# Kernel optimization log

Hardware: AMD Instinct MI355X
Metric: run time of the kernel (lower is better)

Reference implementation:

```python
import jax, jax.numpy as jnp
import numpy as np

NQ = 100000  # Query nodes
NP = 100000  # Product nodes
E = 600000   # edges per relation
D_IN = 128
D_H = 128
# relation r: (src_type, dst_type); 0=Query, 1=Product
# 0: Click Q->P, 1: reverse_Click P->Q, 2: reverse_QueryResult P->Q, 3: QueryResult Q->P
REL = [(0, 1), (1, 0), (1, 0), (0, 1)]
N_NODES = [NQ, NP]


def setup_inputs() -> dict:
    key = jax.random.key(0)
    ks = jax.random.split(key, 12)
    s = 1.0 / np.sqrt(D_IN)  # keep activations well-scaled across 2 layers
    return {
        "x_query": jax.random.normal(ks[0], (NQ, D_IN), jnp.float32),
        "x_product": jax.random.normal(ks[1], (NP, D_IN), jnp.float32),
        "src_idx": jax.random.randint(ks[2], (4, E), 0, NQ, jnp.int32),
        "dst_idx": jax.random.randint(ks[3], (4, E), 0, NP, jnp.int32),
        "W_self1": jax.random.normal(ks[4], (4, D_IN, D_H), jnp.float32) * s,
        "W_neigh1": jax.random.normal(ks[5], (4, D_IN, D_H), jnp.float32) * s,
        "b1": jnp.zeros((4, D_H), jnp.float32),
        "W_self2": jax.random.normal(ks[6], (4, D_H, D_H), jnp.float32) * s,
        "W_neigh2": jax.random.normal(ks[7], (4, D_H, D_H), jnp.float32) * s,
        "b2": jnp.zeros((4, D_H), jnp.float32),
    }


def _hetero_sage_layer(h, W_self, W_neigh, b, src_idx, dst_idx):
    # h: [h_query, h_product]; per-relation SAGEConv(mean), cross-relation sum
    acc = [None, None]
    for r, (s, t) in enumerate(REL):
        nt = N_NODES[t]
        msg = h[s][src_idx[r]]                                   # [E, d] gather
        neigh_sum = jax.ops.segment_sum(msg, dst_idx[r], num_segments=nt)
        deg = jax.ops.segment_sum(jnp.ones((E,), h[s].dtype), dst_idx[r],
                                  num_segments=nt)
        neigh_mean = neigh_sum / jnp.maximum(deg, 1.0)[:, None]
        out = h[t] @ W_self[r] + neigh_mean @ W_neigh[r] + b[r]
        acc[t] = out if acc[t] is None else acc[t] + out
    return acc


def reference(x_query, x_product, src_idx, dst_idx,
              W_self1, W_neigh1, b1, W_self2, W_neigh2, b2):
    h = [x_query, x_product]
    h = _hetero_sage_layer(h, W_self1, W_neigh1, b1, src_idx, dst_idx)
    h = [jax.nn.relu(v) for v in h]  # ReLU only between layers
    h = _hetero_sage_layer(h, W_self2, W_neigh2, b2, src_idx, dst_idx)
    return (h[0], h[1])  # (H_query, H_product)
```

## Files before the change

### kernel.cpp

```cpp
#include <hip/hip_runtime.h>
#include <hip/hip_bf16.h>

#define N_NODES 100000
#define NEDGE   600000
#define SCAN_B  1024
#define NBLK    98
#define BSHIFT  9
#define NBUCK   196
#define BCAP    3456

typedef __attribute__((ext_vector_type(8))) short bf16x8;
typedef __attribute__((ext_vector_type(4))) short s16x4;
typedef __attribute__((ext_vector_type(4))) float f32x4;
typedef __attribute__((ext_vector_type(4))) unsigned u32x4;
typedef __attribute__((ext_vector_type(2))) int int2v;

__device__ __forceinline__ short f2bf(float f) {
  union { float f; unsigned u; } x; x.f = f;
  unsigned r = x.u + 0x7FFFu + ((x.u >> 16) & 1u);
  return (short)(r >> 16);
}

__global__ __launch_bounds__(256) void bin_k(const int* __restrict__ sidx,
                                             const int* __restrict__ didx,
                                             int* __restrict__ bincnt,
                                             int2v* __restrict__ stage) {
  __shared__ int hist[NBUCK];
  __shared__ int base[NBUCK];
  int r = blockIdx.y, t = threadIdx.x;
  int e0 = blockIdx.x * 2048 + t;
  const int* dd = didx + (size_t)r * NEDGE;
  const int* ss = sidx + (size_t)r * NEDGE;
  for (int i = t; i < NBUCK; i += 256) hist[i] = 0;
  __syncthreads();
  int sv[8], dv[8], bu[8], lr[8];
#pragma unroll
  for (int j = 0; j < 8; ++j) {
    int e = e0 + j * 256;
    if (e < NEDGE) {
      dv[j] = dd[e]; sv[j] = ss[e];
      bu[j] = dv[j] >> BSHIFT;
      lr[j] = atomicAdd(&hist[bu[j]], 1);
    }
  }
  __syncthreads();
  for (int i = t; i < NBUCK; i += 256)
    base[i] = atomicAdd(&bincnt[r * NBUCK + i], hist[i]);
  __syncthreads();
#pragma unroll
  for (int j = 0; j < 8; ++j) {
    int e = e0 + j * 256;
    if (e < NEDGE)
      stage[(size_t)(r * NBUCK + bu[j]) * BCAP + base[bu[j]] + lr[j]] =
          (int2v){sv[j], dv[j]};
  }
}

__global__ __launch_bounds__(256) void hist_k(const int2v* __restrict__ stage,
                                              const int* __restrict__ bincnt,
                                              int* __restrict__ cnt) {
  __shared__ int h[512];
  int bu = blockIdx.x, r = blockIdx.y, t = threadIdx.x;
  int len = bincnt[r * NBUCK + bu];
  const int2v* sg = stage + (size_t)(r * NBUCK + bu) * BCAP;
  h[t] = 0; h[t + 256] = 0;
  __syncthreads();
  int lo = bu << BSHIFT;
  for (int i = t; i < len; i += 256) atomicAdd(&h[sg[i].y - lo], 1);
  __syncthreads();
  int d0 = lo + t;
  if (d0 < N_NODES)       cnt[r * N_NODES + d0]       = h[t];
  if (d0 + 256 < N_NODES) cnt[r * N_NODES + d0 + 256] = h[t + 256];
}

__global__ __launch_bounds__(256) void scan1_k(const int* __restrict__ cnt,
                                               int* __restrict__ bsum) {
  __shared__ int lds[256];
  int b = blockIdx.x, r = blockIdx.y, t = threadIdx.x;
  int i0 = b * SCAN_B + t * 4;
  int s = 0;
#pragma unroll
  for (int j = 0; j < 4; ++j)
    if (i0 + j < N_NODES) s += cnt[r * N_NODES + i0 + j];
  lds[t] = s;
  __syncthreads();
  for (int st = 128; st > 0; st >>= 1) {
    if (t < st) lds[t] += lds[t + st];
    __syncthreads();
  }
  if (t == 0) bsum[r * NBLK + b] = lds[0];
}

__global__ __launch_bounds__(128) void scan2_k(int* __restrict__ bsum) {
  __shared__ int buf[128];
  int t = threadIdx.x;
  for (int r = 0; r < 4; ++r) {
    int v = (t < NBLK) ? bsum[r * NBLK + t] : 0;
    buf[t] = v;
    __syncthreads();
    for (int st = 1; st < 128; st <<= 1) {
      int x = (t >= st) ? buf[t - st] : 0;
      __syncthreads();
      buf[t] += x;
      __syncthreads();
    }
    if (t < NBLK) bsum[r * NBLK + t] = buf[t] - v;
    __syncthreads();
  }
}

__global__ __launch_bounds__(256) void scan3_k(const int* __restrict__ cnt,
                                               const int* __restrict__ bsum,
                                               int* __restrict__ off) {
  __shared__ int lds[256];
  int b = blockIdx.x, r = blockIdx.y, t = threadIdx.x;
  int i0 = b * SCAN_B + t * 4;
  int c[4] = {0, 0, 0, 0};
#pragma unroll
  for (int j = 0; j < 4; ++j)
    if (i0 + j < N_NODES) c[j] = cnt[r * N_NODES + i0 + j];
  int s = c[0] + c[1] + c[2] + c[3];
  lds[t] = s;
  __syncthreads();
  for (int st = 1; st < 256; st <<= 1) {
    int x = (t >= st) ? lds[t - st] : 0;
    __syncthreads();
    lds[t] += x;
    __syncthreads();
  }
  int run = bsum[r * NBLK + b] + lds[t] - s;
  int* o = off + r * (N_NODES + 1);
#pragma unroll
  for (int j = 0; j < 4; ++j) {
    if (i0 + j < N_NODES) { o[i0 + j] = run; run += c[j]; }
  }
  if (b == 0 && t == 0) o[N_NODES] = NEDGE;
}

__global__ __launch_bounds__(256) void place_k(const int2v* __restrict__ stage,
                                               const int* __restrict__ bincnt,
                                               const int* __restrict__ off,
                                               int* __restrict__ csr) {
  __shared__ int ofl[512];
  __shared__ int cur[512];
  int bu = blockIdx.x, r = blockIdx.y, t = threadIdx.x;
  int len = bincnt[r * NBUCK + bu];
  const int2v* sg = stage + (size_t)(r * NBUCK + bu) * BCAP;
  const int* of = off + r * (N_NODES + 1);
  int* cs = csr + (size_t)r * NEDGE;
  int lo = bu << BSHIFT;
  int d0 = lo + t;
  ofl[t]       = (d0 < N_NODES) ? of[d0] : 0;
  ofl[t + 256] = (d0 + 256 < N_NODES) ? of[d0 + 256] : 0;
  cur[t] = 0; cur[t + 256] = 0;
  __syncthreads();
  for (int i = t; i < len; i += 256) {
    int2v sd = sg[i];
    int dl = sd.y - lo;
    int pos = ofl[dl] + atomicAdd(&cur[dl], 1);
    cs[pos] = sd.x;
  }
}

__global__ __launch_bounds__(256) void cvt_bf16_k(const float* __restrict__ x,
                                                  unsigned* __restrict__ o) {
  int i = blockIdx.x * 256 + threadIdx.x;
  if (i >= N_NODES * 16) return;
  f32x4 v0 = ((const f32x4*)x)[i * 2];
  f32x4 v1 = ((const f32x4*)x)[i * 2 + 1];
  unsigned r0 = (unsigned)(unsigned short)f2bf(v0[0]) |
                ((unsigned)(unsigned short)f2bf(v0[1]) << 16);
  unsigned r1 = (unsigned)(unsigned short)f2bf(v0[2]) |
                ((unsigned)(unsigned short)f2bf(v0[3]) << 16);
  unsigned r2 = (unsigned)(unsigned short)f2bf(v1[0]) |
                ((unsigned)(unsigned short)f2bf(v1[1]) << 16);
  unsigned r3 = (unsigned)(unsigned short)f2bf(v1[2]) |
                ((unsigned)(unsigned short)f2bf(v1[3]) << 16);
  ((u32x4*)o)[i] = (u32x4){r0, r1, r2, r3};
}

__global__ __launch_bounds__(256) void prep_w_k(const float* __restrict__ Ws1,
                                                const float* __restrict__ Wn1,
                                                const float* __restrict__ Ws2,
                                                const float* __restrict__ Wn2,
                                                short* __restrict__ WTp) {
  int tid = blockIdx.x * 256 + threadIdx.x;
  int lane = tid & 63;
  int n0 = (tid >> 6) & 7;
  int idx3 = tid >> 9;
  int k0 = idx3 % 12;
  int lt = idx3 / 12;
  int l = lt >> 1, t = lt & 1;
  const float* Wself  = l ? Ws2 : Ws1;
  const float* Wneigh = l ? Wn2 : Wn1;
  int rA = t ? 0 : 1, rB = t ? 3 : 2;
  int n = n0 * 16 + (lane & 15);
  int kbase = k0 * 32 + (lane >> 4) * 8;
  short out[8];
#pragma unroll
  for (int j = 0; j < 8; ++j) {
    int k = kbase + j;
    int kk = k & 127, blk = k >> 7;
    float v;
    if (blk == 0)      v = Wself[rA * 16384 + kk * 128 + n] + Wself[rB * 16384 + kk * 128 + n];
    else if (blk == 1) v = Wneigh[rA * 16384 + kk * 128 + n];
    else               v = Wneigh[rB * 16384 + kk * 128 + n];
    out[j] = f2bf(v);
  }
  s16x4* dst = (s16x4*)&WTp[tid * 8];
  dst[0] = *(s16x4*)&out[0];
  dst[1] = *(s16x4*)&out[4];
}

__global__ __launch_bounds__(256) void prep_b_k(const float* __restrict__ b1,
                                                const float* __restrict__ b2,
                                                float* __restrict__ biasc) {
  int tid = blockIdx.x * 256 + threadIdx.x;
  if (tid >= 512) return;
  int l = tid >> 8, t = (tid >> 7) & 1, c = tid & 127;
  const float* b = l ? b2 : b1;
  int rA = t ? 0 : 1, rB = t ? 3 : 2;
  biasc[tid] = b[rA * 128 + c] + b[rB * 128 + c];
}

__global__ __launch_bounds__(256) void gather_mean_k(const unsigned* __restrict__ src,
    const int* __restrict__ csrA, const int* __restrict__ offA,
    const int* __restrict__ csrB, const int* __restrict__ offB,
    unsigned* __restrict__ meanA, unsigned* __restrict__ meanB) {
  int wv = __builtin_amdgcn_readfirstlane(threadIdx.x >> 6);
  int wid = blockIdx.x * 4 + wv;
  int lane = threadIdx.x & 63;
  int n = wid >> 1, rel = wid & 1;
  if (n >= N_NODES) return;
  const int* csr = rel ? csrB : csrA;
  const int* off = rel ? offB : offA;
  unsigned* mean = rel ? meanB : meanA;
  int p0 = off[n], p1 = off[n + 1];
  int deg = p1 - p0;
  int rowg = lane >> 4;
  int colg = lane & 15;
  float a[8] = {};
  for (int p = p0; p < p1; p += 8) {
    int pc0 = p + rowg, pc1 = p + 4 + rowg;
    int i0 = csr[pc0 < p1 ? pc0 : p0];
    int i1 = csr[pc1 < p1 ? pc1 : p0];
    u32x4 u0 = *(const u32x4*)(src + (size_t)i0 * 64 + colg * 4);
    u32x4 u1 = *(const u32x4*)(src + (size_t)i1 * 64 + colg * 4);
    if (pc0 < p1) {
#pragma unroll
      for (int q = 0; q < 4; ++q) {
        union { unsigned w; float f; } lo, hi;
        lo.w = u0[q] << 16; hi.w = u0[q] & 0xffff0000u;
        a[2 * q] += lo.f; a[2 * q + 1] += hi.f;
      }
    }
    if (pc1 < p1) {
#pragma unroll
      for (int q = 0; q < 4; ++q) {
        union { unsigned w; float f; } lo, hi;
        lo.w = u1[q] << 16; hi.w = u1[q] & 0xffff0000u;
        a[2 * q] += lo.f; a[2 * q + 1] += hi.f;
      }
    }
  }
#pragma unroll
  for (int q = 0; q < 8; ++q) {
    a[q] += __shfl_xor(a[q], 16);
    a[q] += __shfl_xor(a[q], 32);
  }
  if (rowg == 0) {
    float inv = 1.0f / (float)(deg > 1 ? deg : 1);
    u32x4 wv4;
#pragma unroll
    for (int q = 0; q < 4; ++q) {
      wv4[q] = (unsigned)(unsigned short)f2bf(a[2 * q] * inv) |
               ((unsigned)(unsigned short)f2bf(a[2 * q + 1] * inv) << 16);
    }
    *(u32x4*)(mean + (size_t)n * 64 + colg * 4) = wv4;
  }
}

template<int OUT_RELU_BF16>
__global__ __launch_bounds__(256) void gemm_k(const short* __restrict__ selfp,
    const short* __restrict__ meanA, const short* __restrict__ meanB,
    const short* __restrict__ WTp, const float* __restrict__ biasc,
    void* __restrict__ outp) {
  __shared__ short Wlds[6 * 8 * 512];
  int tid = threadIdx.x;
  int lane = tid & 63, wave = tid >> 6;
  int rowbase = blockIdx.x * 128 + wave * 32;
  int r0 = rowbase + (lane & 15), r1 = r0 + 16;
  int rc0 = r0 < N_NODES ? r0 : N_NODES - 1;
  int rc1 = r1 < N_NODES ? r1 : N_NODES - 1;
  int kg = lane >> 4;
  f32x4 acc[2][8] = {};
  for (int half = 0; half < 2; ++half) {
    __syncthreads();
    const f32x4* s = (const f32x4*)WTp + half * 3072;
    f32x4* dst = (f32x4*)Wlds;
#pragma unroll
    for (int i = 0; i < 12; ++i) dst[tid + i * 256] = s[tid + i * 256];
    __syncthreads();
    for (int k0h = 0; k0h < 6; ++k0h) {
      int k0 = half * 6 + k0h;
      int kin = (k0 & 3) * 32 + kg * 8;
      const short* mp = (k0 < 4) ? selfp : ((k0 < 8) ? meanA : meanB);
      bf16x8 a0 = *(const bf16x8*)(mp + (size_t)rc0 * 128 + kin);
      bf16x8 a1 = *(const bf16x8*)(mp + (size_t)rc1 * 128 + kin);
      const short* wb = &Wlds[k0h * 4096 + lane * 8];
#pragma unroll
      for (int n0 = 0; n0 < 8; ++n0) {
        bf16x8 b = *(const bf16x8*)(wb + n0 * 512);
        acc[0][n0] = __builtin_amdgcn_mfma_f32_16x16x32_bf16(a0, b, acc[0][n0], 0, 0, 0);
        acc[1][n0] = __builtin_amdgcn_mfma_f32_16x16x32_bf16(a1, b, acc[1][n0], 0, 0, 0);
      }
    }
  }
  int colb = lane & 15, rloc = kg * 4;
#pragma unroll
  for (int mt = 0; mt < 2; ++mt) {
    int rb = rowbase + mt * 16 + rloc;
#pragma unroll
    for (int n0 = 0; n0 < 8; ++n0) {
      int cc = n0 * 16 + colb;
      float bv = biasc[cc];
#pragma unroll
      for (int j = 0; j < 4; ++j) {
        int rr = rb + j;
        if (rr < N_NODES) {
          float v = acc[mt][n0][j] + bv;
          if (OUT_RELU_BF16) {
            ((short*)outp)[(size_t)rr * 128 + cc] = f2bf(v > 0.f ? v : 0.f);
          } else {
            ((float*)outp)[(size_t)rr * 128 + cc] = v;
          }
        }
      }
    }
  }
}

extern "C" void kernel_launch(void* const* d_in, const int* in_sizes, int n_in,
                              void* d_out, int out_size, void* d_ws, size_t ws_size,
                              hipStream_t stream) {
  (void)in_sizes; (void)n_in; (void)out_size; (void)ws_size;
  const float* xq  = (const float*)d_in[0];
  const float* xp  = (const float*)d_in[1];
  const int*   src = (const int*)d_in[2];
  const int*   dst = (const int*)d_in[3];
  const float* Ws1 = (const float*)d_in[4];
  const float* Wn1 = (const float*)d_in[5];
  const float* b1  = (const float*)d_in[6];
  const float* Ws2 = (const float*)d_in[7];
  const float* Wn2 = (const float*)d_in[8];
  const float* b2  = (const float*)d_in[9];

  char* w = (char*)d_ws;
  int*   cnt    = (int*)w;      w += (size_t)4 * N_NODES * 4;
  int*   bincnt = (int*)w;      w += 4096;
  int*   off    = (int*)w;      w += (size_t)4 * (N_NODES + 1) * 4;
  int*   csr    = (int*)w;      w += (size_t)4 * NEDGE * 4;
  short* meanA  = (short*)w;    w += (size_t)N_NODES * 128 * 2;
  short* meanB  = (short*)w;    w += (size_t)N_NODES * 128 * 2;
  short* h1q    = (short*)w;    w += (size_t)N_NODES * 128 * 2;
  short* h1p    = (short*)w;    w += (size_t)N_NODES * 128 * 2;
  short* xqb    = (short*)w;    w += (size_t)N_NODES * 128 * 2;
  short* xpb    = (short*)w;    w += (size_t)N_NODES * 128 * 2;
  short* WTp    = (short*)w;    w += (size_t)4 * 49152 * 2;
  float* biasc  = (float*)w;    w += 512 * 4;
  int*   bsum   = (int*)w;      w += 4 * 128 * 4;
  int2v* stage  = (int2v*)meanA;

  dim3 b256(256);
  const int bgrid = (NEDGE + 2047) / 2048;
  const int ggrid = (N_NODES + 127) / 128;
  const int wgrid = (2 * N_NODES + 3) / 4;
  const int cgrid = (N_NODES * 16 + 255) / 256;
  const int NP1 = N_NODES + 1;

  hipMemsetAsync(bincnt, 0, 4096, stream);
  bin_k<<<dim3(bgrid, 4), b256, 0, stream>>>(src, dst, bincnt, stage);
  hist_k<<<dim3(NBUCK, 4), b256, 0, stream>>>(stage, bincnt, cnt);
  scan1_k<<<dim3(NBLK, 4), b256, 0, stream>>>(cnt, bsum);
  scan2_k<<<dim3(1), dim3(128), 0, stream>>>(bsum);
  scan3_k<<<dim3(NBLK, 4), b256, 0, stream>>>(cnt, bsum, off);
  place_k<<<dim3(NBUCK, 4), b256, 0, stream>>>(stage, bincnt, off, csr);
  prep_w_k<<<dim3(384), b256, 0, stream>>>(Ws1, Wn1, Ws2, Wn2, WTp);
  prep_b_k<<<dim3(2), b256, 0, stream>>>(b1, b2, biasc);
  cvt_bf16_k<<<dim3(cgrid), b256, 0, stream>>>(xq, (unsigned*)xqb);
  cvt_bf16_k<<<dim3(cgrid), b256, 0, stream>>>(xp, (unsigned*)xpb);

  gather_mean_k<<<wgrid, b256, 0, stream>>>((const unsigned*)xpb,
      csr + 1 * NEDGE, off + 1 * NP1, csr + 2 * NEDGE, off + 2 * NP1,
      (unsigned*)meanA, (unsigned*)meanB);
  gemm_k<1><<<ggrid, b256, 0, stream>>>(xqb, meanA, meanB,
      WTp + 0 * 49152, biasc + 0, h1q);

  gather_mean_k<<<wgrid, b256, 0, stream>>>((const unsigned*)xqb,
      csr + 0 * NEDGE, off + 0 * NP1, csr + 3 * NEDGE, off + 3 * NP1,
      (unsigned*)meanA, (unsigned*)meanB);
  gemm_k<1><<<ggrid, b256, 0, stream>>>(xpb, meanA, meanB,
      WTp + 1 * 49152, biasc + 128, h1p);

  gather_mean_k<<<wgrid, b256, 0, stream>>>((const unsigned*)h1p,
      csr + 1 * NEDGE, off + 1 * NP1, csr + 2 * NEDGE, off + 2 * NP1,
      (unsigned*)meanA, (unsigned*)meanB);
  gemm_k<0><<<ggrid, b256, 0, stream>>>(h1q, meanA, meanB,
      WTp + 2 * 49152, biasc + 256, (float*)d_out);

  gather_mean_k<<<wgrid, b256, 0, stream>>>((const unsigned*)h1q,
      csr + 0 * NEDGE, off + 0 * NP1, csr + 3 * NEDGE, off + 3 * NP1,
      (unsigned*)meanA, (unsigned*)meanB);
  gemm_k<0><<<ggrid, b256, 0, stream>>>(h1p, meanA, meanB,
      WTp + 3 * 49152, biasc + 384, (float*)d_out + (size_t)N_NODES * 128);
}
```

Measured before the change: 544.0 us.

## Batch both node types per layer into single gather and GEMM launches

```diff
diff --git a/kernel.cpp b/kernel.cpp
--- a/kernel.cpp
+++ b/kernel.cpp
@@ -162,8 +162,12 @@
   }
 }
 
-__global__ __launch_bounds__(256) void cvt_bf16_k(const float* __restrict__ x,
-                                                  unsigned* __restrict__ o) {
+__global__ __launch_bounds__(256) void cvt2_k(const float* __restrict__ x0,
+                                              const float* __restrict__ x1,
+                                              unsigned* __restrict__ o0,
+                                              unsigned* __restrict__ o1) {
+  const float* x = blockIdx.y ? x1 : x0;
+  unsigned* o = blockIdx.y ? o1 : o0;
   int i = blockIdx.x * 256 + threadIdx.x;
   if (i >= N_NODES * 16) return;
   f32x4 v0 = ((const f32x4*)x)[i * 2];
@@ -223,69 +227,109 @@
   biasc[tid] = b[rA * 128 + c] + b[rB * 128 + c];
 }
 
-__global__ __launch_bounds__(256) void gather_mean_k(const unsigned* __restrict__ src,
-    const int* __restrict__ csrA, const int* __restrict__ offA,
-    const int* __restrict__ csrB, const int* __restrict__ offB,
-    unsigned* __restrict__ meanA, unsigned* __restrict__ meanB) {
+#define ACC8(u, a)                                            \
+  {                                                           \
+    _Pragma("unroll") for (int q = 0; q < 4; ++q) {           \
+      union { unsigned w; float f; } lo_, hi_;                \
+      lo_.w = (u)[q] << 16; hi_.w = (u)[q] & 0xffff0000u;     \
+      (a)[2 * q] += lo_.f; (a)[2 * q + 1] += hi_.f;           \
+    }                                                         \
+  }
+
+__device__ __forceinline__ int clampi(int q, int p0, int p1) {
+  int t = q < p1 ? q : p0;
+  return t < NEDGE ? t : 0;
+}
+
+__global__ __launch_bounds__(256) void gather2_k(
+    const unsigned* __restrict__ src0, const unsigned* __restrict__ src1,
+    const int* __restrict__ csr, const int* __restrict__ off,
+    unsigned* __restrict__ m00, unsigned* __restrict__ m01,
+    unsigned* __restrict__ m10, unsigned* __restrict__ m11) {
   int wv = __builtin_amdgcn_readfirstlane(threadIdx.x >> 6);
   int wid = blockIdx.x * 4 + wv;
   int lane = threadIdx.x & 63;
-  int n = wid >> 1, rel = wid & 1;
-  if (n >= N_NODES) return;
-  const int* csr = rel ? csrB : csrA;
-  const int* off = rel ? offB : offA;
-  unsigned* mean = rel ? meanB : meanA;
-  int p0 = off[n], p1 = off[n + 1];
-  int deg = p1 - p0;
+  int type = wid >= N_NODES;
+  int n = type ? wid - N_NODES : wid;
+  const unsigned* src = type ? src1 : src0;
+  const int* csrA = csr + (type ? 0 : 1) * NEDGE;
+  const int* csrB = csr + (type ? 3 : 2) * NEDGE;
+  const int* offA = off + (type ? 0 : 1) * (N_NODES + 1);
+  const int* offB = off + (type ? 3 : 2) * (N_NODES + 1);
+  unsigned* mA = type ? m10 : m00;
+  unsigned* mB = type ? m11 : m01;
+  int pA0 = offA[n], pA1 = offA[n + 1];
+  int pB0 = offB[n], pB1 = offB[n + 1];
+  int degA = pA1 - pA0, degB = pB1 - pB0;
   int rowg = lane >> 4;
   int colg = lane & 15;
-  float a[8] = {};
-  for (int p = p0; p < p1; p += 8) {
-    int pc0 = p + rowg, pc1 = p + 4 + rowg;
-    int i0 = csr[pc0 < p1 ? pc0 : p0];
-    int i1 = csr[pc1 < p1 ? pc1 : p0];
+  float a[8] = {}, b[8] = {};
+  {
+    int ia0 = csrA[clampi(pA0 + rowg,     pA0, pA1)];
+    int ia1 = csrA[clampi(pA0 + 4 + rowg, pA0, pA1)];
+    int ib0 = csrB[clampi(pB0 + rowg,     pB0, pB1)];
+    int ib1 = csrB[clampi(pB0 + 4 + rowg, pB0, pB1)];
+    u32x4 ua0 = *(const u32x4*)(src + (size_t)ia0 * 64 + colg * 4);
+    u32x4 ua1 = *(const u32x4*)(src + (size_t)ia1 * 64 + colg * 4);
+    u32x4 ub0 = *(const u32x4*)(src + (size_t)ib0 * 64 + colg * 4);
+    u32x4 ub1 = *(const u32x4*)(src + (size_t)ib1 * 64 + colg * 4);
+    if (pA0 + rowg     < pA1) ACC8(ua0, a);
+    if (pA0 + 4 + rowg < pA1) ACC8(ua1, a);
+    if (pB0 + rowg     < pB1) ACC8(ub0, b);
+    if (pB0 + 4 + rowg < pB1) ACC8(ub1, b);
+  }
+  for (int p = pA0 + 8; p < pA1; p += 8) {
+    int i0 = csrA[clampi(p + rowg,     pA0, pA1)];
+    int i1 = csrA[clampi(p + 4 + rowg, pA0, pA1)];
     u32x4 u0 = *(const u32x4*)(src + (size_t)i0 * 64 + colg * 4);
     u32x4 u1 = *(const u32x4*)(src + (size_t)i1 * 64 + colg * 4);
-    if (pc0 < p1) {
-#pragma unroll
-      for (int q = 0; q < 4; ++q) {
-        union { unsigned w; float f; } lo, hi;
-        lo.w = u0[q] << 16; hi.w = u0[q] & 0xffff0000u;
-        a[2 * q] += lo.f; a[2 * q + 1] += hi.f;
-      }
+    if (p + rowg     < pA1) ACC8(u0, a);
+    if (p + 4 + rowg < pA1) ACC8(u1, a);
+  }
+  for (int p = pB0 + 8; p < pB1; p += 8) {
+    int i0 = csrB[clampi(p + rowg,     pB0, pB1)];
+    int i1 = csrB[clampi(p + 4 + rowg, pB0, pB1)];
+    u32x4 u0 = *(const u32x4*)(src + (size_t)i0 * 64 + colg * 4);
+    u32x4 u1 = *(const u32x4*)(src + (size_t)i1 * 64 + colg * 4);
+    if (p + rowg     < pB1) ACC8(u0, b);
+    if (p + 4 + rowg < pB1) ACC8(u1, b);
+  }
+#pragma unroll
+  for (int q = 0; q < 8; ++q) {
+    a[q] += __shfl_xor(a[q], 16); a[q] += __shfl_xor(a[q], 32);
+    b[q] += __shfl_xor(b[q], 16); b[q] += __shfl_xor(b[q], 32);
+  }
+  if (rowg == 0) {
+    float invA = 1.0f / (float)(degA > 1 ? degA : 1);
+    float invB = 1.0f / (float)(degB > 1 ? degB : 1);
+    u32x4 wa, wb;
+#pragma unroll
+    for (int q = 0; q < 4; ++q) {
+      wa[q] = (unsigned)(unsigned short)f2bf(a[2 * q] * invA) |
+              ((unsigned)(unsigned short)f2bf(a[2 * q + 1] * invA) << 16);
+      wb[q] = (unsigned)(unsigned short)f2bf(b[2 * q] * invB) |
+              ((unsigned)(unsigned short)f2bf(b[2 * q + 1] * invB) << 16);
     }
-    if (pc1 < p1) {
-#pragma unroll
-      for (int q = 0; q < 4; ++q) {
-        union { unsigned w; float f; } lo, hi;
-        lo.w = u1[q] << 16; hi.w = u1[q] & 0xffff0000u;
-        a[2 * q] += lo.f; a[2 * q + 1] += hi.f;
-      }
-    }
-  }
-#pragma unroll
-  for (int q = 0; q < 8; ++q) {
-    a[q] += __shfl_xor(a[q], 16);
-    a[q] += __shfl_xor(a[q], 32);
-  }
-  if (rowg == 0) {
-    float inv = 1.0f / (float)(deg > 1 ? deg : 1);
-    u32x4 wv4;
-#pragma unroll
-    for (int q = 0; q < 4; ++q) {
-      wv4[q] = (unsigned)(unsigned short)f2bf(a[2 * q] * inv) |
-               ((unsigned)(unsigned short)f2bf(a[2 * q + 1] * inv) << 16);
-    }
-    *(u32x4*)(mean + (size_t)n * 64 + colg * 4) = wv4;
+    *(u32x4*)(mA + (size_t)n * 64 + colg * 4) = wa;
+    *(u32x4*)(mB + (size_t)n * 64 + colg * 4) = wb;
   }
 }
 
 template<int OUT_RELU_BF16>
-__global__ __launch_bounds__(256) void gemm_k(const short* __restrict__ selfp,
-    const short* __restrict__ meanA, const short* __restrict__ meanB,
-    const short* __restrict__ WTp, const float* __restrict__ biasc,
-    void* __restrict__ outp) {
+__global__ __launch_bounds__(256) void gemm2_k(
+    const short* __restrict__ self0, const short* __restrict__ self1,
+    const short* __restrict__ mA0, const short* __restrict__ mB0,
+    const short* __restrict__ mA1, const short* __restrict__ mB1,
+    const short* __restrict__ WTpL, const float* __restrict__ biascL,
+    void* __restrict__ out0, void* __restrict__ out1) {
   __shared__ short Wlds[6 * 8 * 512];
+  int type = blockIdx.y;
+  const short* selfp = type ? self1 : self0;
+  const short* meanA = type ? mA1 : mA0;
+  const short* meanB = type ? mB1 : mB0;
+  const short* WTp = WTpL + type * 49152;
+  const float* biasc = biascL + type * 128;
+  void* outp = type ? out1 : out0;
   int tid = threadIdx.x;
   int lane = tid & 63, wave = tid >> 6;
   int rowbase = blockIdx.x * 128 + wave * 32;
@@ -370,13 +414,16 @@
   float* biasc  = (float*)w;    w += 512 * 4;
   int*   bsum   = (int*)w;      w += 4 * 128 * 4;
   int2v* stage  = (int2v*)meanA;
+  unsigned* mL1C = (unsigned*)d_out;
+  unsigned* mL1D = mL1C + (size_t)N_NODES * 64;
+  unsigned* mL2C = (unsigned*)xqb;
+  unsigned* mL2D = (unsigned*)xpb;
 
   dim3 b256(256);
   const int bgrid = (NEDGE + 2047) / 2048;
   const int ggrid = (N_NODES + 127) / 128;
-  const int wgrid = (2 * N_NODES + 3) / 4;
+  const int wgrid = 2 * N_NODES / 4;
   const int cgrid = (N_NODES * 16 + 255) / 256;
-  const int NP1 = N_NODES + 1;
 
   hipMemsetAsync(bincnt, 0, 4096, stream);
   bin_k<<<dim3(bgrid, 4), b256, 0, stream>>>(src, dst, bincnt, stage);
@@ -387,30 +434,18 @@
   place_k<<<dim3(NBUCK, 4), b256, 0, stream>>>(stage, bincnt, off, csr);
   prep_w_k<<<dim3(384), b256, 0, stream>>>(Ws1, Wn1, Ws2, Wn2, WTp);
   prep_b_k<<<dim3(2), b256, 0, stream>>>(b1, b2, biasc);
-  cvt_bf16_k<<<dim3(cgrid), b256, 0, stream>>>(xq, (unsigned*)xqb);
-  cvt_bf16_k<<<dim3(cgrid), b256, 0, stream>>>(xp, (unsigned*)xpb);
-
-  gather_mean_k<<<wgrid, b256, 0, stream>>>((const unsigned*)xpb,
-      csr + 1 * NEDGE, off + 1 * NP1, csr + 2 * NEDGE, off + 2 * NP1,
-      (unsigned*)meanA, (unsigned*)meanB);
-  gemm_k<1><<<ggrid, b256, 0, stream>>>(xqb, meanA, meanB,
-      WTp + 0 * 49152, biasc + 0, h1q);
-
-  gather_mean_k<<<wgrid, b256, 0, stream>>>((const unsigned*)xqb,
-      csr + 0 * NEDGE, off + 0 * NP1, csr + 3 * NEDGE, off + 3 * NP1,
-      (unsigned*)meanA, (unsigned*)meanB);
-  gemm_k<1><<<ggrid, b256, 0, stream>>>(xpb, meanA, meanB,
-      WTp + 1 * 49152, biasc + 128, h1p);
-
-  gather_mean_k<<<wgrid, b256, 0, stream>>>((const unsigned*)h1p,
-      csr + 1 * NEDGE, off + 1 * NP1, csr + 2 * NEDGE, off + 2 * NP1,
-      (unsigned*)meanA, (unsigned*)meanB);
-  gemm_k<0><<<ggrid, b256, 0, stream>>>(h1q, meanA, meanB,
-      WTp + 2 * 49152, biasc + 256, (float*)d_out);
-
-  gather_mean_k<<<wgrid, b256, 0, stream>>>((const unsigned*)h1q,
-      csr + 0 * NEDGE, off + 0 * NP1, csr + 3 * NEDGE, off + 3 * NP1,
-      (unsigned*)meanA, (unsigned*)meanB);
-  gemm_k<0><<<ggrid, b256, 0, stream>>>(h1p, meanA, meanB,
-      WTp + 3 * 49152, biasc + 384, (float*)d_out + (size_t)N_NODES * 128);
-}
+  cvt2_k<<<dim3(cgrid, 2), b256, 0, stream>>>(xq, xp, (unsigned*)xqb, (unsigned*)xpb);
+
+  gather2_k<<<wgrid, b256, 0, stream>>>((const unsigned*)xpb, (const unsigned*)xqb,
+      csr, off, (unsigned*)meanA, (unsigned*)meanB, mL1C, mL1D);
+  gemm2_k<1><<<dim3(ggrid, 2), b256, 0, stream>>>(
+      xqb, xpb, meanA, meanB, (const short*)mL1C, (const short*)mL1D,
+      WTp, biasc, h1q, h1p);
+
+  gather2_k<<<wgrid, b256, 0, stream>>>((const unsigned*)h1p, (const unsigned*)h1q,
+      csr, off, (unsigned*)meanA, (unsigned*)meanB, mL2C, mL2D);
+  gemm2_k<0><<<dim3(ggrid, 2), b256, 0, stream>>>(
+      h1q, h1p, meanA, meanB, (const short*)mL2C, (const short*)mL2D,
+      WTp + 2 * 49152, biasc + 256,
+      (float*)d_out, (float*)d_out + (size_t)N_NODES * 128);
+}
```

After: 471.9 us. 1.15x faster.
